# Kernel tuning notes

Hardware: AMD Instinct MI355X
Metric: run time of the kernel (lower is better)

The kernel has to match this reference:

```python
import jax, jax.numpy as jnp
import numpy as np

W_REG = 3.0
N_CAND = 4
IOU_LEN = 15.0
BIG_COST = 1e8


def focal_cost(cls_pred, gt_labels, alpha=0.25, gamma=2.0, eps=1e-12):
    # cls_pred: [B,P,C] logits, gt_labels: [B,T] int -> [B,P,T]
    p = jax.nn.sigmoid(cls_pred)
    neg = -jnp.log(1.0 - p + eps) * (1.0 - alpha) * p ** gamma
    pos = -jnp.log(p + eps) * alpha * (1.0 - p) ** gamma
    B, P, _ = cls_pred.shape
    T = gt_labels.shape[1]
    idx = jnp.broadcast_to(gt_labels[:, None, :], (B, P, T))
    return jnp.take_along_axis(pos, idx, axis=2) - jnp.take_along_axis(neg, idx, axis=2)


def line_iou(pred, target, img_w, length=IOU_LEN):
    # pred: [B,P,O], target: [B,T,O] -> [B,P,T] (unaligned)
    px1, px2 = pred - length, pred + length
    tx1, tx2 = target - length, target + length
    ovr = jnp.minimum(px2[:, :, None, :], tx2[:, None, :, :]) - jnp.maximum(px1[:, :, None, :], tx1[:, None, :, :])
    union = jnp.maximum(px2[:, :, None, :], tx2[:, None, :, :]) - jnp.minimum(px1[:, :, None, :], tx1[:, None, :, :])
    invalid = ((target < 0) | (target >= img_w))[:, None, :, :]
    ovr = jnp.where(invalid, 0.0, ovr)
    union = jnp.where(invalid, 0.0, union)
    return ovr.sum(-1) / (union.sum(-1) + 1e-9)


def clrnet_assign(preds, targets, masks, img_w, img_h):
    B, P, _ = preds.shape
    T = targets.shape[1]
    w = float(img_w - 1)
    h = float(img_h - 1)
    pa = preds.at[..., 3].multiply(w).at[..., 6:].multiply(w)
    ta = targets.at[..., 3].multiply(w).at[..., 6:].multiply(w)
    p_off, t_off = pa[..., 6:], ta[..., 6:]

    # --- distance score (masked mean L1 over valid target x-offsets) ---
    tvalid = (t_off >= 0) & (t_off < img_w)                      # [B,T,O]
    cmask = tvalid[:, None, :, :]                                 # [B,1,T,O]
    clen = jnp.maximum(cmask.sum(-1).astype(pa.dtype), 1.0)      # [B,1,T]
    diff = jnp.abs(p_off[:, :, None, :] - t_off[:, None, :, :]) * cmask  # [B,P,T,O]
    distances = diff.sum(-1) / clen                               # [B,P,T]
    dist_max = jnp.maximum(distances.max(axis=(1, 2), keepdims=True), 1e-8)
    dist_score = 1.0 - distances / dist_max + 0.01

    # --- start-point score (euclidean on (y*(h), x)) ---
    ps = pa[..., 2:4].at[..., 0].multiply(h)
    ts = ta[..., 2:4].at[..., 0].multiply(h)
    start_d = jnp.sqrt(((ps[:, :, None, :] - ts[:, None, :, :]) ** 2).sum(-1))
    start_max = jnp.maximum(start_d.max(axis=(1, 2), keepdims=True), 1e-8)
    start_score = 1.0 - start_d / start_max + 0.01

    # --- theta score ---
    th_d = jnp.abs(pa[..., 4][:, :, None] - ta[..., 4][:, None, :]) * 180.0
    th_max = jnp.maximum(th_d.max(axis=(1, 2), keepdims=True), 1e-8)
    th_score = 1.0 - th_d / th_max + 0.01

    # --- total cost ---
    gt_labels = ta[..., 1].astype(jnp.int32)
    cls_cost = focal_cost(pa[..., :2], gt_labels)
    reg = (jnp.maximum(dist_score, 1e-3) * jnp.maximum(start_score, 1e-3)
           * jnp.maximum(th_score, 1e-3))
    total_cost = -(reg ** 2) * W_REG + cls_cost                   # [B,P,T]
    valid_t = (masks > 0)[:, None, :]                             # [B,1,T]
    total_cost = jnp.where(valid_t, total_cost, BIG_COST)

    # --- dynamic-k from line IoU ---
    liou = jnp.nan_to_num(line_iou(p_off, t_off, img_w), nan=0.0)
    liou = jnp.where(valid_t, liou, 0.0)
    k = min(N_CAND, P)
    topk_ious, _ = jax.lax.top_k(jnp.swapaxes(liou, 1, 2), k)     # [B,T,k]
    dynamic_ks = jnp.maximum(topk_ious.sum(-1).astype(jnp.int32), 1)
    dynamic_ks = jnp.where(masks > 0, dynamic_ks, 0)              # [B,T]

    # --- top-k lowest-cost priors per target, scatter into matching matrix ---
    _, topk_idx = jax.lax.top_k(-jnp.swapaxes(total_cost, 1, 2), k)  # [B,T,k]
    sel = (jnp.arange(k)[None, None, :] < dynamic_ks[:, :, None]).astype(total_cost.dtype)  # [B,T,k]
    one_hot_p = jax.nn.one_hot(topk_idx, P, dtype=total_cost.dtype)  # [B,T,k,P]
    matching = jnp.swapaxes((one_hot_p * sel[..., None]).sum(2), 1, 2)  # [B,P,T]

    # --- conflict resolution: a prior matched to >1 targets keeps argmin-cost one ---
    conflict = matching.sum(-1) > 1                               # [B,P]
    masked_cost = jnp.where(matching == 0, jnp.inf, total_cost)
    best_t = jnp.argmin(masked_cost, axis=2)                      # [B,P]
    new_m = jax.nn.one_hot(best_t, T, dtype=matching.dtype)
    matching = jnp.where(conflict[..., None], new_m, matching)

    has_match = matching.sum(-1) > 0.5
    t_idx = jnp.argmax(matching, axis=2)
    matched = jnp.where(has_match, t_idx, -1).astype(jnp.int32)
    return matched >= 0, matched


def setup_inputs() -> dict:
    key = jax.random.key(0)
    k1, k2, k3 = jax.random.split(key, 3)
    B, P, T, O = 32, 1000, 16, 72
    D = 6 + O
    preds = jax.random.uniform(k1, (B, P, D), dtype=jnp.float32)
    # slightly outside [0,1] so the invalid-offset masking path is exercised
    targets = jax.random.uniform(k2, (B, T, D), dtype=jnp.float32, minval=-0.05, maxval=1.05)
    masks = jax.random.randint(k3, (B, T), 0, 2).astype(jnp.int32)
    return {"preds": preds, "targets": targets, "masks": masks, "img_w": 800, "img_h": 320}


def reference(preds, targets, masks, img_w, img_h):
    return clrnet_assign(preds, targets, masks, img_w, img_h)
```

## Files before the change

### kernel.cpp

```cpp
#include <hip/hip_runtime.h>
#include <math.h>

#define B_ 32
#define P_ 1000
#define T_ 16
#define D_ 78
#define O_ 72
#define NXB 16
#define BIGC 100000000.0f

__global__ __launch_bounds__(1024, 8) void k1(
        const float* __restrict__ preds, const float* __restrict__ targets,
        const int* __restrict__ imgw_p, const int* __restrict__ imgh_p,
        float* __restrict__ Sarr, float4* __restrict__ scal4, float* __restrict__ pths,
        float* __restrict__ pmax, float* __restrict__ cntg) {
    __shared__ float pred_s[64 * 81];
    __shared__ float2 tomg[T_ * O_];
    __shared__ float Spart[T_][4][64];
    __shared__ float wmax[16][3];
    __shared__ float cnt_s[T_], clen_s[T_], ts0_s[T_], ts1_s[T_], tth_s[T_];

    const int b = blockIdx.y, bx = blockIdx.x;
    const int p0 = bx * 64;
    const int rows = min(64, P_ - p0);
    const int tid = threadIdx.x;
    const float w = (float)(imgw_p[0] - 1);
    const float h = (float)(imgh_p[0] - 1);
    const float imgwf = (float)imgw_p[0];

    {
        const float4* gbase = (const float4*)(preds + ((size_t)b * P_ + p0) * D_);
        const int n4 = rows * D_ / 4;
        for (int i = tid; i < n4; i += 1024) {
            float4 v = gbase[i];
            int base = i * 4;
            int r = base / D_, c = base - r * D_;
#pragma unroll
            for (int k = 0; k < 4; ++k) {
                int cc = c + k, rr = r;
                if (cc >= D_) { cc -= D_; ++rr; }
                float x = (&v.x)[k];
                if (cc >= 6 || cc == 3) x *= w;
                pred_s[rr * 81 + cc] = x;
            }
        }
    }
    for (int i = tid; i < T_ * O_; i += 1024) {
        int t = i / O_, o = i - t * O_;
        float to = targets[((size_t)b * T_ + t) * D_ + 6 + o] * w;
        float m = (to >= 0.f && to < imgwf) ? 1.f : 0.f;
        tomg[((t >> 2) * O_ + o) * 4 + (t & 3)] = make_float2(to, m);
    }
    __syncthreads();
    if (tid < T_) {
        int t = tid;
        float c = 0.f;
        for (int o = 0; o < O_; ++o) c += tomg[((t >> 2) * O_ + o) * 4 + (t & 3)].y;
        cnt_s[t] = c;
        clen_s[t] = fmaxf(c, 1.f);
        const float* tr = targets + ((size_t)b * T_ + t) * D_;
        ts0_s[t] = tr[2] * h;
        ts1_s[t] = tr[3] * w;
        tth_s[t] = tr[4];
    }
    __syncthreads();

    if (bx == 0 && tid < T_) cntg[b * T_ + tid] = cnt_s[tid];

    {
        const int lane = tid & 63;
        const int wv = tid >> 6;
        const int tg = wv & 3;
        const int oq = wv >> 2;
        const float* lrow = pred_s + lane * 81;
        const float4* tg4 = (const float4*)(tomg + (size_t)tg * O_ * 4);
        const int o_lo = oq * 18;
        float S0 = 0.f, S1 = 0.f, S2 = 0.f, S3 = 0.f;
#pragma unroll
        for (int i = 0; i < 18; ++i) {
            int o = o_lo + i;
            float po = lrow[6 + o];
            float4 r0 = tg4[2 * o];
            float4 r1 = tg4[2 * o + 1];
            S0 += r0.y * fabsf(po - r0.x);
            S1 += r0.w * fabsf(po - r0.z);
            S2 += r1.y * fabsf(po - r1.x);
            S3 += r1.w * fabsf(po - r1.z);
        }
        Spart[4 * tg + 0][oq][lane] = S0;
        Spart[4 * tg + 1][oq][lane] = S1;
        Spart[4 * tg + 2][oq][lane] = S2;
        Spart[4 * tg + 3][oq][lane] = S3;
    }
    __syncthreads();

    const int th = tid >> 6, pl = tid & 63;
    const int p = p0 + pl;
    float ldm = 0.f, lsm = 0.f, ltm = 0.f;
    if (pl < rows) {
        float S = ((Spart[th][0][pl] + Spart[th][1][pl]) + Spart[th][2][pl]) + Spart[th][3][pl];
        Sarr[(size_t)(b * T_ + th) * P_ + p] = S;
        float dv = S / clen_s[th];
        ldm = dv;
        const float* prow = pred_s + pl * 81;
        float ps0 = prow[2] * h, ps1 = prow[3], pth = prow[4];
        float d0 = ps0 - ts0_s[th], d1 = ps1 - ts1_s[th];
        lsm = sqrtf(d0 * d0 + d1 * d1);
        ltm = fabsf(pth - tth_s[th]) * 180.f;
        if (th == 0) {
            float fc[2];
#pragma unroll
            for (int c = 0; c < 2; ++c) {
                float x = prow[c];
                float pc = 1.f / (1.f + expf(-x));
                float neg = -logf(1.f - pc + 1e-12f) * 0.75f * pc * pc;
                float pos = -logf(pc + 1e-12f) * 0.25f * (1.f - pc) * (1.f - pc);
                fc[c] = pos - neg;
            }
            scal4[(size_t)b * P_ + p] = make_float4(fc[0], fc[1], ps0, ps1);
            pths[(size_t)b * P_ + p] = pth;
        }
    }

    for (int off = 32; off; off >>= 1) {
        ldm = fmaxf(ldm, __shfl_xor(ldm, off, 64));
        lsm = fmaxf(lsm, __shfl_xor(lsm, off, 64));
        ltm = fmaxf(ltm, __shfl_xor(ltm, off, 64));
    }
    if (pl == 0) { wmax[th][0] = ldm; wmax[th][1] = lsm; wmax[th][2] = ltm; }
    __syncthreads();
    if (tid == 0) {
        float m0 = 0.f, m1 = 0.f, m2 = 0.f;
#pragma unroll
        for (int i = 0; i < 16; ++i) {
            m0 = fmaxf(m0, wmax[i][0]);
            m1 = fmaxf(m1, wmax[i][1]);
            m2 = fmaxf(m2, wmax[i][2]);
        }
        float* q = pmax + (size_t)(b * NXB + bx) * 3;
        q[0] = m0; q[1] = m1; q[2] = m2;
    }
}

__global__ __launch_bounds__(256) void k2(
        const float* __restrict__ targets, const int* __restrict__ masks,
        const int* __restrict__ imgw_p, const int* __restrict__ imgh_p,
        const float* __restrict__ Sarr,
        const float4* __restrict__ scal4, const float* __restrict__ pths,
        const float* __restrict__ pmax, const float* __restrict__ cntg,
        int4* __restrict__ sel, float4* __restrict__ selc) {
    __shared__ float costL[1024];
    __shared__ float SL[1024];

    const int wid = blockIdx.x;
    const int b = wid >> 4, t = wid & 15;
    const int tid = threadIdx.x;

    float dm = 0.f, sm = 0.f, tm = 0.f;
    for (int i = 0; i < NXB; ++i) {
        const float* q = pmax + (size_t)(b * NXB + i) * 3;
        dm = fmaxf(dm, q[0]); sm = fmaxf(sm, q[1]); tm = fmaxf(tm, q[2]);
    }
    dm = fmaxf(dm, 1e-8f); sm = fmaxf(sm, 1e-8f); tm = fmaxf(tm, 1e-8f);

    const float w = (float)(imgw_p[0] - 1);
    const float h = (float)(imgh_p[0] - 1);
    const float* tr = targets + (size_t)(b * T_ + t) * D_;
    const float ts0 = tr[2] * h, ts1 = tr[3] * w, tth = tr[4];
    int lab = (int)tr[1]; lab = lab < 0 ? 0 : (lab > 1 ? 1 : lab);
    const int mk = masks[b * T_ + t];
    const float cntv = cntg[b * T_ + t];
    const float clen = fmaxf(cntv, 1.f);
    const float c30 = 30.f * cntv;

    const float* Srow = Sarr + (size_t)(b * T_ + t) * P_;
    const float4* s4b = scal4 + (size_t)b * P_;
    const float* ptb = pths + (size_t)b * P_;

#pragma unroll
    for (int i = 0; i < 4; ++i) {
        int p = tid + 256 * i;
        if (p < P_) {
            float S = Srow[p];
            float4 s4 = s4b[p];
            float pth = ptb[p];
            float dv = S / clen;
            float dsc = 1.f - dv / dm + 0.01f;
            float d0 = s4.z - ts0, d1 = s4.w - ts1;
            float ssc = 1.f - sqrtf(d0 * d0 + d1 * d1) / sm + 0.01f;
            float tsc = 1.f - fabsf(pth - tth) * 180.f / tm + 0.01f;
            float reg = fmaxf(dsc, 1e-3f) * fmaxf(ssc, 1e-3f) * fmaxf(tsc, 1e-3f);
            float c = -(reg * reg) * 3.f + (lab ? s4.y : s4.x);
            if (mk <= 0) c = BIGC;
            costL[p] = c;
            SL[p] = S;
        } else {
            costL[p] = INFINITY;
            SL[p] = INFINITY;
        }
    }
    __syncthreads();
    if (tid >= 64) return;

    const int lane = tid;

    float v0, v1, v2, v3;
#define SROUND(vr) { float bv = INFINITY; int bi = 0x7fffffff;            \
        _Pragma("unroll")                                                 \
        for (int i = 0; i < 16; ++i) { int ix = lane + 64 * i;            \
            float v = SL[ix];                                             \
            if (v < bv || (v == bv && ix < bi)) { bv = v; bi = ix; } }    \
        for (int off = 32; off; off >>= 1) {                              \
            float ov = __shfl_xor(bv, off, 64);                           \
            int oi = __shfl_xor(bi, off, 64);                             \
            if (ov < bv || (ov == bv && oi < bi)) { bv = ov; bi = oi; }   \
        }                                                                 \
        vr = bv; if ((bi & 63) == lane) SL[bi] = INFINITY; }
    SROUND(v0) SROUND(v1) SROUND(v2) SROUND(v3)
#undef SROUND
    float l0 = (c30 - v0) / (c30 + v0 + 1e-9f);
    float l1 = (c30 - v1) / (c30 + v1 + 1e-9f);
    float l2 = (c30 - v2) / (c30 + v2 + 1e-9f);
    float l3 = (c30 - v3) / (c30 + v3 + 1e-9f);
    float sum = ((l0 + l1) + l2) + l3;
    int dk = 0;
    if (mk > 0) {
        dk = (int)sum;
        if (dk < 1) dk = 1;
        if (dk > 4) dk = 4;
    }

    int s0, s1, s2, s3;
    float c0, c1, c2, c3;
#define CROUND(sr, cr) { float bv = INFINITY; int bi = 0x7fffffff;        \
        _Pragma("unroll")                                                 \
        for (int i = 0; i < 16; ++i) { int ix = lane + 64 * i;            \
            float v = costL[ix];                                          \
            if (v < bv || (v == bv && ix < bi)) { bv = v; bi = ix; } }    \
        for (int off = 32; off; off >>= 1) {                              \
            float ov = __shfl_xor(bv, off, 64);                           \
            int oi = __shfl_xor(bi, off, 64);                             \
            if (ov < bv || (ov == bv && oi < bi)) { bv = ov; bi = oi; }   \
        }                                                                 \
        sr = bi; cr = bv; if ((bi & 63) == lane) costL[bi] = INFINITY; }
    CROUND(s0, c0) CROUND(s1, c1) CROUND(s2, c2) CROUND(s3, c3)
#undef CROUND

    if (lane == 0) {
        sel[wid]  = make_int4(dk > 0 ? s0 : -1, dk > 1 ? s1 : -1,
                              dk > 2 ? s2 : -1, dk > 3 ? s3 : -1);
        selc[wid] = make_float4(c0, c1, c2, c3);
    }
}

__global__ __launch_bounds__(256) void k3(const int* __restrict__ sel,
                                          const float* __restrict__ selc,
                                          int* __restrict__ out) {
    __shared__ int selE[64];
    __shared__ float selC[64];
    const int b = blockIdx.y, cx = blockIdx.x;
    if (threadIdx.x < 64) {
        selE[threadIdx.x] = sel[b * 64 + threadIdx.x];
        selC[threadIdx.x] = selc[b * 64 + threadIdx.x];
    }
    __syncthreads();

    const int p = cx * 250 + threadIdx.x;
    if (threadIdx.x < 250) {
        int matched = -1;
        float best = INFINITY;
#pragma unroll
        for (int t = 0; t < T_; ++t) {
#pragma unroll
            for (int j = 0; j < 4; ++j) {
                if (selE[4 * t + j] == p) {
                    float c = selC[4 * t + j];
                    if (c < best) { best = c; matched = t; }
                }
            }
        }
        out[b * P_ + p] = (matched >= 0) ? 1 : 0;
        out[B_ * P_ + b * P_ + p] = matched;
    }
}

extern "C" void kernel_launch(void* const* d_in, const int* in_sizes, int n_in,
                              void* d_out, int out_size, void* d_ws, size_t ws_size,
                              hipStream_t stream) {
    const float* preds   = (const float*)d_in[0];
    const float* targets = (const float*)d_in[1];
    const int*   masks   = (const int*)d_in[2];
    const int*   imgw    = (const int*)d_in[3];
    const int*   imgh    = (const int*)d_in[4];
    int* out = (int*)d_out;

    char* ws = (char*)d_ws;
    float*  Sarr  = (float*)ws;
    float4* scal4 = (float4*)(ws + 2048000);
    float*  pths  = (float*)(ws + 2560000);
    float*  pmax  = (float*)(ws + 2688000);
    float*  cntg  = (float*)(ws + 2694144);
    int4*   sel   = (int4*)(ws + 2696192);
    float4* selc  = (float4*)(ws + 2704384);

    k1<<<dim3(NXB, B_), 1024, 0, stream>>>(preds, targets, imgw, imgh,
                                           Sarr, scal4, pths, pmax, cntg);
    k2<<<B_ * T_, 256, 0, stream>>>(targets, masks, imgw, imgh, Sarr, scal4, pths,
                                    pmax, cntg, sel, selc);
    k3<<<dim3(4, B_), 256, 0, stream>>>((const int*)sel, (const float*)selc, out);
}
```

Before: 34.28 us.

## Shrink k1 to 256 threads with full offset loop per thread

Result: slower. 35.38 us (+3.2%).

```diff
diff --git a/kernel.cpp b/kernel.cpp
--- a/kernel.cpp
+++ b/kernel.cpp
@@ -9,15 +9,14 @@
 #define NXB 16
 #define BIGC 100000000.0f
 
-__global__ __launch_bounds__(1024, 8) void k1(
+__global__ __launch_bounds__(256) void k1(
         const float* __restrict__ preds, const float* __restrict__ targets,
         const int* __restrict__ imgw_p, const int* __restrict__ imgh_p,
         float* __restrict__ Sarr, float4* __restrict__ scal4, float* __restrict__ pths,
         float* __restrict__ pmax, float* __restrict__ cntg) {
     __shared__ float pred_s[64 * 81];
     __shared__ float2 tomg[T_ * O_];
-    __shared__ float Spart[T_][4][64];
-    __shared__ float wmax[16][3];
+    __shared__ float wmax[4][3];
     __shared__ float cnt_s[T_], clen_s[T_], ts0_s[T_], ts1_s[T_], tth_s[T_];
 
     const int b = blockIdx.y, bx = blockIdx.x;
@@ -31,7 +30,7 @@
     {
         const float4* gbase = (const float4*)(preds + ((size_t)b * P_ + p0) * D_);
         const int n4 = rows * D_ / 4;
-        for (int i = tid; i < n4; i += 1024) {
+        for (int i = tid; i < n4; i += 256) {
             float4 v = gbase[i];
             int base = i * 4;
             int r = base / D_, c = base - r * D_;
@@ -45,7 +44,7 @@
             }
         }
     }
-    for (int i = tid; i < T_ * O_; i += 1024) {
+    for (int i = tid; i < T_ * O_; i += 256) {
         int t = i / O_, o = i - t * O_;
         float to = targets[((size_t)b * T_ + t) * D_ + 6 + o] * w;
         float m = (to >= 0.f && to < imgwf) ? 1.f : 0.f;
@@ -67,18 +66,17 @@
 
     if (bx == 0 && tid < T_) cntg[b * T_ + tid] = cnt_s[tid];
 
-    {
-        const int lane = tid & 63;
-        const int wv = tid >> 6;
-        const int tg = wv & 3;
-        const int oq = wv >> 2;
+    const int lane = tid & 63;
+    const int tg = tid >> 6;
+    const int p = p0 + lane;
+
+    float ldm = 0.f, lsm = 0.f, ltm = 0.f;
+    if (p < P_) {
         const float* lrow = pred_s + lane * 81;
         const float4* tg4 = (const float4*)(tomg + (size_t)tg * O_ * 4);
-        const int o_lo = oq * 18;
         float S0 = 0.f, S1 = 0.f, S2 = 0.f, S3 = 0.f;
-#pragma unroll
-        for (int i = 0; i < 18; ++i) {
-            int o = o_lo + i;
+#pragma unroll 4
+        for (int o = 0; o < O_; ++o) {
             float po = lrow[6 + o];
             float4 r0 = tg4[2 * o];
             float4 r1 = tg4[2 * o + 1];
@@ -87,31 +85,24 @@
             S2 += r1.y * fabsf(po - r1.x);
             S3 += r1.w * fabsf(po - r1.z);
         }
-        Spart[4 * tg + 0][oq][lane] = S0;
-        Spart[4 * tg + 1][oq][lane] = S1;
-        Spart[4 * tg + 2][oq][lane] = S2;
-        Spart[4 * tg + 3][oq][lane] = S3;
-    }
-    __syncthreads();
-
-    const int th = tid >> 6, pl = tid & 63;
-    const int p = p0 + pl;
-    float ldm = 0.f, lsm = 0.f, ltm = 0.f;
-    if (pl < rows) {
-        float S = ((Spart[th][0][pl] + Spart[th][1][pl]) + Spart[th][2][pl]) + Spart[th][3][pl];
-        Sarr[(size_t)(b * T_ + th) * P_ + p] = S;
-        float dv = S / clen_s[th];
-        ldm = dv;
-        const float* prow = pred_s + pl * 81;
-        float ps0 = prow[2] * h, ps1 = prow[3], pth = prow[4];
-        float d0 = ps0 - ts0_s[th], d1 = ps1 - ts1_s[th];
-        lsm = sqrtf(d0 * d0 + d1 * d1);
-        ltm = fabsf(pth - tth_s[th]) * 180.f;
-        if (th == 0) {
+        float Sv[4] = {S0, S1, S2, S3};
+        float ps0 = lrow[2] * h, ps1 = lrow[3], pth = lrow[4];
+#pragma unroll
+        for (int j = 0; j < 4; ++j) {
+            int t = 4 * tg + j;
+            float S = Sv[j];
+            Sarr[(size_t)(b * T_ + t) * P_ + p] = S;
+            float dv = S / clen_s[t];
+            ldm = fmaxf(ldm, dv);
+            float d0 = ps0 - ts0_s[t], d1 = ps1 - ts1_s[t];
+            lsm = fmaxf(lsm, sqrtf(d0 * d0 + d1 * d1));
+            ltm = fmaxf(ltm, fabsf(pth - tth_s[t]) * 180.f);
+        }
+        if (tg == 0) {
             float fc[2];
 #pragma unroll
             for (int c = 0; c < 2; ++c) {
-                float x = prow[c];
+                float x = lrow[c];
                 float pc = 1.f / (1.f + expf(-x));
                 float neg = -logf(1.f - pc + 1e-12f) * 0.75f * pc * pc;
                 float pos = -logf(pc + 1e-12f) * 0.25f * (1.f - pc) * (1.f - pc);
@@ -127,12 +118,12 @@
         lsm = fmaxf(lsm, __shfl_xor(lsm, off, 64));
         ltm = fmaxf(ltm, __shfl_xor(ltm, off, 64));
     }
-    if (pl == 0) { wmax[th][0] = ldm; wmax[th][1] = lsm; wmax[th][2] = ltm; }
+    if (lane == 0) { wmax[tg][0] = ldm; wmax[tg][1] = lsm; wmax[tg][2] = ltm; }
     __syncthreads();
     if (tid == 0) {
         float m0 = 0.f, m1 = 0.f, m2 = 0.f;
 #pragma unroll
-        for (int i = 0; i < 16; ++i) {
+        for (int i = 0; i < 4; ++i) {
             m0 = fmaxf(m0, wmax[i][0]);
             m1 = fmaxf(m1, wmax[i][1]);
             m2 = fmaxf(m2, wmax[i][2]);
@@ -303,8 +294,8 @@
     int4*   sel   = (int4*)(ws + 2696192);
     float4* selc  = (float4*)(ws + 2704384);
 
-    k1<<<dim3(NXB, B_), 1024, 0, stream>>>(preds, targets, imgw, imgh,
-                                           Sarr, scal4, pths, pmax, cntg);
+    k1<<<dim3(NXB, B_), 256, 0, stream>>>(preds, targets, imgw, imgh,
+                                          Sarr, scal4, pths, pmax, cntg);
     k2<<<B_ * T_, 256, 0, stream>>>(targets, masks, imgw, imgh, Sarr, scal4, pths,
                                     pmax, cntg, sel, selc);
     k3<<<dim3(4, B_), 256, 0, stream>>>((const int*)sel, (const float*)selc, out);
```
